# Optimization experiments

Hardware: AMD Instinct MI355X
Metric: run time of the kernel (lower is better)

The kernel has to match this reference:

```python
import jax, jax.numpy as jnp
import numpy as np

NEG_SLOPE = 0.2


def _gat(x, src, dst, W, a_src, a_dst, b, N):
    # PyG GATConv (eval mode, concat=True). W: [Fin, H*C], a_*: [H, C], b: [H*C]
    H, C = a_src.shape
    h = (x @ W).reshape(N, H, C)                       # [N,H,C]
    al_s = jnp.einsum('nhc,hc->nh', h, a_src)          # source attention logits
    al_d = jnp.einsum('nhc,hc->nh', h, a_dst)          # target attention logits
    e = jax.nn.leaky_relu(al_s[src] + al_d[dst], NEG_SLOPE)  # [E,H]
    m = jax.ops.segment_max(e, dst, num_segments=N)
    m = jnp.where(jnp.isneginf(m), 0.0, m)
    p = jnp.exp(e - m[dst])
    s = jax.ops.segment_sum(p, dst, num_segments=N)
    alpha = p / (s[dst] + 1e-16)                       # segment softmax over incoming edges
    out = jax.ops.segment_sum(h[src] * alpha[:, :, None], dst, num_segments=N)
    return out.reshape(N, H * C) + b


def _lin(key, fin, fout):
    k1, k2 = jax.random.split(key)
    w = jax.random.normal(k1, (fin, fout), jnp.float32) / np.sqrt(fin)
    b = jax.random.normal(k2, (fout,), jnp.float32) * 0.01
    return w, b


def _gat_params(key, fin, H, C):
    k1, k2, k3, k4 = jax.random.split(key, 4)
    W = jax.random.normal(k1, (fin, H * C), jnp.float32) / np.sqrt(fin)
    a_s = jax.random.normal(k2, (H, C), jnp.float32) / np.sqrt(C)
    a_d = jax.random.normal(k3, (H, C), jnp.float32) / np.sqrt(C)
    b = jax.random.normal(k4, (H * C,), jnp.float32) * 0.01
    return W, a_s, a_d, b


def setup_inputs() -> dict:
    key = jax.random.key(0)
    N, E, F, HID, H = 20000, 320000, 128, 128, 2
    W_ = HID * H  # 256
    ks = jax.random.split(key, 12)
    x = jax.random.normal(ks[0], (N, F), jnp.float32)
    edge_index = jax.random.randint(ks[1], (2, E), 0, N, jnp.int64)
    edge_attr = jax.random.normal(ks[2], (E, 4), jnp.float32)
    ec_w1, ec_b1 = _lin(ks[3], 2 * F, HID)
    ec_w2, ec_b2 = _lin(ks[4], HID, HID)
    g1 = _gat_params(ks[5], HID, H, HID)
    g2 = _gat_params(ks[6], W_, H, HID)
    reg_w, reg_b = _lin(ks[7], W_, W_)
    g3 = _gat_params(ks[8], W_, H, HID)
    g4 = _gat_params(ks[9], W_, H, HID)
    fin_w, fin_b = _lin(ks[10], W_, 1)
    d = {"x": x, "edge_index": edge_index, "edge_attr": edge_attr,
         "ec_w1": ec_w1, "ec_b1": ec_b1, "ec_w2": ec_w2, "ec_b2": ec_b2,
         "reg_w": reg_w, "reg_b": reg_b, "fin_w": fin_w, "fin_b": fin_b}
    for name, p in (("g1", g1), ("g2", g2), ("g3", g3), ("g4", g4)):
        d[name + "_w"], d[name + "_as"], d[name + "_ad"], d[name + "_b"] = p
    return d


def reference(x, edge_index, edge_attr,
              ec_w1, ec_b1, ec_w2, ec_b2,
              g1_w, g1_as, g1_ad, g1_b,
              g2_w, g2_as, g2_ad, g2_b,
              reg_w, reg_b,
              g3_w, g3_as, g3_ad, g3_b,
              g4_w, g4_as, g4_ad, g4_b,
              fin_w, fin_b):
    N = x.shape[0]
    src, dst = edge_index[0], edge_index[1]
    # EdgeConv: msg = MLP([x_i, x_j - x_i]), max-aggregation at target i (no self loops)
    xi = x[dst]
    msg = jnp.concatenate([xi, x[src] - xi], axis=-1)          # [E, 2F]
    h = jnp.maximum(msg @ ec_w1 + ec_b1, 0.0) @ ec_w2 + ec_b2   # [E, HID]
    agg = jax.ops.segment_max(h, dst, num_segments=N)
    x = jnp.where(jnp.isneginf(agg), 0.0, agg)
    # GATConv adds self loops by default
    loop = jnp.arange(N, dtype=src.dtype)
    s2 = jnp.concatenate([src, loop])
    d2 = jnp.concatenate([dst, loop])
    # edge_attr is ignored by GATConv (edge_dim=None)
    x = jax.nn.relu(_gat(x, s2, d2, g1_w, g1_as, g1_ad, g1_b, N))
    r = x
    x = jax.nn.relu(_gat(x, s2, d2, g2_w, g2_as, g2_ad, g2_b, N)) + r
    x = x @ reg_w + reg_b
    r = x
    x = jax.nn.relu(_gat(x, s2, d2, g3_w, g3_as, g3_ad, g3_b, N)) + r
    x = jax.nn.relu(_gat(x, s2, d2, g4_w, g4_as, g4_ad, g4_b, N))
    return x @ fin_w + fin_b
```

## Files before the change

kernel.cpp:

```cpp
#include <hip/hip_runtime.h>
#include <math.h>


#define NEG_SLOPE 0.2f

typedef short short8 __attribute__((ext_vector_type(8)));
typedef float float4v __attribute__((ext_vector_type(4)));
typedef unsigned short ushort4v __attribute__((ext_vector_type(4)));

#define AS1 __attribute__((address_space(1)))
#define AS3 __attribute__((address_space(3)))

__device__ __forceinline__ void cp16(const void* g, void* l) {
  __builtin_amdgcn_global_load_lds((const AS1 unsigned int*)g, (AS3 unsigned int*)l, 16, 0, 0);
}

__device__ __forceinline__ float leaky(float x) { return x > 0.f ? x : NEG_SLOPE * x; }

__device__ __forceinline__ void atomicMaxF(float* addr, float v) {
  if (v >= 0.f) atomicMax((int*)addr, __float_as_int(v));
  else          atomicMin((unsigned int*)addr, __float_as_uint(v));
}

__device__ __forceinline__ unsigned short bf16_rn(float f) {
  unsigned u = __float_as_uint(f);
  unsigned r = (u + 0x7FFFu + ((u >> 16) & 1u)) >> 16;
  return (unsigned short)r;
}
__device__ __forceinline__ float bf16_to_f(unsigned short h) {
  return __uint_as_float(((unsigned)h) << 16);
}

__global__ __launch_bounds__(256) void k_fill_f32(float* p, float v, int n) {
  int i = blockIdx.x * 256 + threadIdx.x;
  if (i < n) p[i] = v;
}

__global__ __launch_bounds__(256) void k_split_act(const float* __restrict__ src,
                                                   unsigned short* __restrict__ h,
                                                   unsigned short* __restrict__ l,
                                                   int n, int fixinf) {
  int i4 = (blockIdx.x * 256 + threadIdx.x) * 4;
  if (i4 >= n) return;
  float4 v = *(const float4*)&src[i4];
  if (fixinf) {
    if (v.x == -INFINITY) v.x = 0.f;
    if (v.y == -INFINITY) v.y = 0.f;
    if (v.z == -INFINITY) v.z = 0.f;
    if (v.w == -INFINITY) v.w = 0.f;
  }
  unsigned short hx = bf16_rn(v.x), hy = bf16_rn(v.y), hz = bf16_rn(v.z), hw = bf16_rn(v.w);
  ushort4v h4 = {hx, hy, hz, hw};
  ushort4v l4 = {bf16_rn(v.x - bf16_to_f(hx)), bf16_rn(v.y - bf16_to_f(hy)),
                 bf16_rn(v.z - bf16_to_f(hz)), bf16_rn(v.w - bf16_to_f(hw))};
  *(ushort4v*)&h[i4] = h4;
  *(ushort4v*)&l[i4] = l4;
}

__global__ __launch_bounds__(256) void k_hist(const int* __restrict__ ei, int* __restrict__ deg,
                                              int E) {
  int e = blockIdx.x * 256 + threadIdx.x;
  if (e < E) atomicAdd(&deg[ei[E + e]], 1);
}

__global__ __launch_bounds__(1024) void k_scan(const int* __restrict__ deg, int* __restrict__ rs,
                                               int n) {
  __shared__ int wsum[16];
  __shared__ int carry;
  int tid = threadIdx.x, lane = tid & 63, wv = tid >> 6;
  if (tid == 0) carry = 0;
  __syncthreads();
  for (int base = 0; base < n; base += 1024) {
    int i = base + tid;
    int v = (i < n) ? deg[i] : 0;
    int s = v;
    #pragma unroll
    for (int o = 1; o < 64; o <<= 1) {
      int t = __shfl(s, lane - o);
      if (lane >= o) s += t;
    }
    if (lane == 63) wsum[wv] = s;
    __syncthreads();
    if (wv == 0) {
      int x = (lane < 16) ? wsum[lane] : 0;
      #pragma unroll
      for (int o = 1; o < 16; o <<= 1) {
        int t = __shfl(x, lane - o);
        if (lane >= o) x += t;
      }
      if (lane < 16) wsum[lane] = x;
    }
    __syncthreads();
    int woff = carry + (wv ? wsum[wv - 1] : 0);
    if (i < n) rs[i] = woff + s - v;
    __syncthreads();
    if (tid == 0) carry += wsum[15];
    __syncthreads();
  }
  if (tid == 0) rs[n] = carry;
}

__global__ __launch_bounds__(256) void k_scatter(const int* __restrict__ ei,
                                                 const int* __restrict__ rs,
                                                 int* __restrict__ cnt,
                                                 int* __restrict__ csr_src,
                                                 int* __restrict__ csr_dst, int E) {
  int e = blockIdx.x * 256 + threadIdx.x;
  if (e < E) {
    int d = ei[E + e];
    int p = atomicAdd(&cnt[d], 1);
    int slot = rs[d] + p;
    csr_src[slot] = ei[e];
    csr_dst[slot] = d;
  }
}

struct SplitJob {
  const float* W;
  const float* aux;
  unsigned short* Th;
  unsigned short* Tl;
  float* bias_out;
  int K, N, kshift, type;
};
struct SplitJobs { SplitJob j[7]; };

__global__ __launch_bounds__(256) void k_prep_all(SplitJobs jobs) {
  SplitJob jb = jobs.j[blockIdx.y];
  int idx = blockIdx.x * 256 + threadIdx.x;
  if (idx >= jb.K * jb.N) return;
  float v;
  if (jb.type == 0) {
    int n = idx >> jb.kshift;
    int k = idx & (jb.K - 1);
    v = jb.W[k * jb.N + n];
  } else {
    int n = idx >> 7;
    int k = idx & 127;
    if (n < 128) v = jb.W[k * 128 + n] - jb.W[(k + 128) * 128 + n];
    else         v = jb.W[(k + 128) * 128 + (n - 128)];
    if (idx < 256) jb.bias_out[idx] = (idx < 128) ? jb.aux[idx] : 0.f;
  }
  unsigned short h = bf16_rn(v);
  jb.Th[idx] = h;
  jb.Tl[idx] = bf16_rn(v - bf16_to_f(h));
}

__global__ __launch_bounds__(256) void k_gemm_mfma(const unsigned short* __restrict__ Ah,
                                                   const unsigned short* __restrict__ Al,
                                                   const unsigned short* __restrict__ BTh,
                                                   const unsigned short* __restrict__ BTl,
                                                   const float* __restrict__ bias,
                                                   float* __restrict__ C, int M, int K,
                                                   unsigned short* __restrict__ Ch,
                                                   unsigned short* __restrict__ Cl,
                                                   const float* __restrict__ a_s,
                                                   const float* __restrict__ a_d,
                                                   float* __restrict__ al_out) {
  __shared__ __align__(16) char sm[24576];
  __shared__ float alS[64][2];
  char* AhS = sm;
  char* AlS = sm + 4096;
  char* BhS = sm + 8192;
  char* BlS = sm + 16384;

  const int tid = threadIdx.x;
  const int bm = blockIdx.x * 64;
  const int bn = blockIdx.y * 128;
  const int w = tid >> 6, lane = tid & 63, quad = lane >> 4, lr = lane & 15;
  const int kq8 = quad * 8;

  float4v zero4 = {0.f, 0.f, 0.f, 0.f};
  float4v acc[4][2];
  #pragma unroll
  for (int mt = 0; mt < 4; ++mt)
    #pragma unroll
    for (int nt = 0; nt < 2; ++nt) acc[mt][nt] = zero4;

  int ar = bm + w * 16 + lr; if (ar >= M) ar = M - 1;
  const size_t aoff  = (size_t)ar * K + kq8;
  const size_t boff0 = (size_t)(bn + (2 * w) * 16 + lr) * K + kq8;
  const size_t boff1 = (size_t)(bn + (2 * w + 1) * 16 + lr) * K + kq8;
  char* lA   = AhS + w * 1024;
  char* lAl  = AlS + w * 1024;
  char* lB0  = BhS + (2 * w) * 1024;
  char* lB1  = BhS + (2 * w + 1) * 1024;
  char* lBl0 = BlS + (2 * w) * 1024;
  char* lBl1 = BlS + (2 * w + 1) * 1024;

  for (int k0 = 0; k0 < K; k0 += 32) {
    __syncthreads();
    cp16(Ah + aoff + k0, lA);
    cp16(Al + aoff + k0, lAl);
    cp16(BTh + boff0 + k0, lB0);
    cp16(BTh + boff1 + k0, lB1);
    cp16(BTl + boff0 + k0, lBl0);
    cp16(BTl + boff1 + k0, lBl1);
    __syncthreads();
    short8 ah[4], alo[4], bh[2], blo[2];
    #pragma unroll
    for (int mt = 0; mt < 4; ++mt) {
      ah[mt]  = *(const short8*)(AhS + mt * 1024 + lane * 16);
      alo[mt] = *(const short8*)(AlS + mt * 1024 + lane * 16);
    }
    #pragma unroll
    for (int nt = 0; nt < 2; ++nt) {
      bh[nt]  = *(const short8*)(BhS + (2 * w + nt) * 1024 + lane * 16);
      blo[nt] = *(const short8*)(BlS + (2 * w + nt) * 1024 + lane * 16);
    }
    #pragma unroll
    for (int mt = 0; mt < 4; ++mt)
      #pragma unroll
      for (int nt = 0; nt < 2; ++nt) {
        acc[mt][nt] = __builtin_amdgcn_mfma_f32_16x16x32_bf16(ah[mt], bh[nt], acc[mt][nt], 0, 0, 0);
        acc[mt][nt] = __builtin_amdgcn_mfma_f32_16x16x32_bf16(alo[mt], bh[nt], acc[mt][nt], 0, 0, 0);
        acc[mt][nt] = __builtin_amdgcn_mfma_f32_16x16x32_bf16(ah[mt], blo[nt], acc[mt][nt], 0, 0, 0);
      }
  }
  #pragma unroll
  for (int nt = 0; nt < 2; ++nt) {
    int n = bn + w * 32 + nt * 16 + lr;
    float bv = bias ? bias[n] : 0.f;
    #pragma unroll
    for (int mt = 0; mt < 4; ++mt) {
      #pragma unroll
      for (int r = 0; r < 4; ++r) {
        int m = bm + mt * 16 + quad * 4 + r;
        if (m < M) {
          float v = acc[mt][nt][r] + bv;
          size_t idx = (size_t)m * 256 + n;
          C[idx] = v;
          if (Ch) {
            unsigned short h = bf16_rn(v);
            Ch[idx] = h;
            Cl[idx] = bf16_rn(v - bf16_to_f(h));
          }
        }
      }
    }
  }
  if (a_s) {
    if (tid < 128) ((float*)alS)[tid] = 0.f;
    __syncthreads();
    float asv[2], adv[2];
    #pragma unroll
    for (int nt = 0; nt < 2; ++nt) {
      int n = bn + w * 32 + nt * 16 + lr;
      asv[nt] = a_s[n];
      adv[nt] = a_d[n];
    }
    #pragma unroll
    for (int mt = 0; mt < 4; ++mt) {
      #pragma unroll
      for (int r = 0; r < 4; ++r) {
        float ps = acc[mt][0][r] * asv[0] + acc[mt][1][r] * asv[1];
        float pd = acc[mt][0][r] * adv[0] + acc[mt][1][r] * adv[1];
        #pragma unroll
        for (int o = 8; o; o >>= 1) {
          ps += __shfl_xor(ps, o);
          pd += __shfl_xor(pd, o);
        }
        if (lr == 0) {
          int row = mt * 16 + quad * 4 + r;
          atomicAdd(&alS[row][0], ps);
          atomicAdd(&alS[row][1], pd);
        }
      }
    }
    __syncthreads();
    int head = bn >> 7;
    if (tid < 64) {
      int m = bm + tid;
      if (m < M) {
        al_out[m * 4 + head]     = alS[tid][0];
        al_out[m * 4 + 2 + head] = alS[tid][1];
      }
    }
  }
}

__global__ __launch_bounds__(256, 4) void k_edgeconv2(const float* __restrict__ uv,
                                                      const int* __restrict__ csr_src,
                                                      const int* __restrict__ csr_dst,
                                                      const unsigned short* __restrict__ w2Th,
                                                      const unsigned short* __restrict__ w2Tl,
                                                      const float* __restrict__ b2,
                                                      float* __restrict__ x0, int E) {
  __shared__ __align__(16) char smem[34816];
  unsigned short (*Ph)[136] = (unsigned short(*)[136])smem;
  unsigned short (*Pl)[136] = (unsigned short(*)[136])(smem + 17408);
  float (*H2)[132] = (float(*)[132])smem;
  __shared__ int sSrc[64], sDst[64];

  const int tid = threadIdx.x;
  const int e0 = blockIdx.x * 64;
  const int w = tid >> 6, lane = tid & 63, quad = lane >> 4, lr = lane & 15;
  if (tid < 64) {
    int e = e0 + tid;
    sSrc[tid] = (e < E) ? csr_src[e] : -1;
    sDst[tid] = (e < E) ? csr_dst[e] : -1;
  }
  __syncthreads();
  #pragma unroll
  for (int c = tid; c < 1024; c += 256) {
    int r = c >> 4;
    int kq = (c & 15) * 8;
    float pv[8];
    int sn = sSrc[r], dn = sDst[r];
    if (sn >= 0) {
      float4 u0 = *(const float4*)&uv[(size_t)dn * 256 + kq];
      float4 u1 = *(const float4*)&uv[(size_t)dn * 256 + kq + 4];
      float4 v0 = *(const float4*)&uv[(size_t)sn * 256 + 128 + kq];
      float4 v1 = *(const float4*)&uv[(size_t)sn * 256 + 128 + kq + 4];
      pv[0] = fmaxf(u0.x + v0.x, 0.f); pv[1] = fmaxf(u0.y + v0.y, 0.f);
      pv[2] = fmaxf(u0.z + v0.z, 0.f); pv[3] = fmaxf(u0.w + v0.w, 0.f);
      pv[4] = fmaxf(u1.x + v1.x, 0.f); pv[5] = fmaxf(u1.y + v1.y, 0.f);
      pv[6] = fmaxf(u1.z + v1.z, 0.f); pv[7] = fmaxf(u1.w + v1.w, 0.f);
    } else {
      #pragma unroll
      for (int i = 0; i < 8; ++i) pv[i] = 0.f;
    }
    short8 h8, l8;
    #pragma unroll
    for (int i = 0; i < 8; ++i) {
      unsigned short h = bf16_rn(pv[i]);
      h8[i] = (short)h;
      l8[i] = (short)bf16_rn(pv[i] - bf16_to_f(h));
    }
    *(short8*)&Ph[r][kq] = h8;
    *(short8*)&Pl[r][kq] = l8;
  }
  __syncthreads();
  float4v zero4 = {0.f, 0.f, 0.f, 0.f};
  float4v acc[4][2];
  #pragma unroll
  for (int mt = 0; mt < 4; ++mt)
    #pragma unroll
    for (int nt = 0; nt < 2; ++nt) acc[mt][nt] = zero4;

  #pragma unroll
  for (int k0 = 0; k0 < 128; k0 += 32) {
    short8 ah[4], alo[4], bh[2], blo[2];
    #pragma unroll
    for (int nt = 0; nt < 2; ++nt) {
      int n = w * 32 + nt * 16 + lr;
      bh[nt]  = *(const short8*)&w2Th[(size_t)n * 128 + k0 + quad * 8];
      blo[nt] = *(const short8*)&w2Tl[(size_t)n * 128 + k0 + quad * 8];
    }
    #pragma unroll
    for (int mt = 0; mt < 4; ++mt) {
      ah[mt]  = *(short8*)&Ph[mt * 16 + lr][k0 + quad * 8];
      alo[mt] = *(short8*)&Pl[mt * 16 + lr][k0 + quad * 8];
    }
    #pragma unroll
    for (int mt = 0; mt < 4; ++mt)
      #pragma unroll
      for (int nt = 0; nt < 2; ++nt) {
        acc[mt][nt] = __builtin_amdgcn_mfma_f32_16x16x32_bf16(ah[mt], bh[nt], acc[mt][nt], 0, 0, 0);
        acc[mt][nt] = __builtin_amdgcn_mfma_f32_16x16x32_bf16(alo[mt], bh[nt], acc[mt][nt], 0, 0, 0);
        acc[mt][nt] = __builtin_amdgcn_mfma_f32_16x16x32_bf16(ah[mt], blo[nt], acc[mt][nt], 0, 0, 0);
      }
  }
  __syncthreads();
  #pragma unroll
  for (int nt = 0; nt < 2; ++nt) {
    int n = w * 32 + nt * 16 + lr;
    float bv = b2[n];
    #pragma unroll
    for (int mt = 0; mt < 4; ++mt) {
      #pragma unroll
      for (int r = 0; r < 4; ++r) {
        int row = mt * 16 + quad * 4 + r;
        H2[row][n] = acc[mt][nt][r] + bv;
      }
    }
  }
  __syncthreads();
  if (tid < 128) {
    int col = tid;
    int prev = sDst[0];
    float rmax = H2[0][col];
    for (int r = 1; r < 64; ++r) {
      int d = sDst[r];
      float v = H2[r][col];
      if (d == prev) {
        rmax = fmaxf(rmax, v);
      } else {
        if (prev >= 0) atomicMaxF(&x0[(size_t)prev * 128 + col], rmax);
        prev = d;
        rmax = v;
      }
    }
    if (prev >= 0) atomicMaxF(&x0[(size_t)prev * 128 + col], rmax);
  }
}

__global__ __launch_bounds__(256) void k_gat_agg(const float* __restrict__ Hf,
                                                 const float* __restrict__ al,
                                                 const int* __restrict__ rs,
                                                 const int* __restrict__ csr_src,
                                                 const float* __restrict__ bias,
                                                 const float* __restrict__ res,
                                                 float* __restrict__ out,
                                                 unsigned short* __restrict__ outh,
                                                 unsigned short* __restrict__ outl,
                                                 const float* __restrict__ finw,
                                                 const float* __restrict__ finb, int N) {
  int wave = threadIdx.x >> 6, lane = threadIdx.x & 63;
  int i = blockIdx.x * 4 + wave;
  if (i >= N) return;
  int beg = rs[i], end = rs[i + 1];
  int deg = end - beg;
  float4 me = *(const float4*)&al[i * 4];
  float ad0 = me.z, ad1 = me.w;
  float sl0 = leaky(me.x + ad0);
  float sl1 = leaky(me.y + ad1);
  const int c = lane << 2;
  const int hsel = lane >> 5;
  float a0, a1, a2, a3;

  if (deg <= 64) {
    int s = 0;
    float l0 = -INFINITY, l1 = -INFINITY;
    bool act = lane < deg;
    if (act) {
      s = csr_src[beg + lane];
      float4 a4 = *(const float4*)&al[s * 4];
      l0 = leaky(a4.x + ad0);
      l1 = leaky(a4.y + ad1);
    }
    float m0 = fmaxf(sl0, l0), m1 = fmaxf(sl1, l1);
    #pragma unroll
    for (int o = 32; o; o >>= 1) {
      m0 = fmaxf(m0, __shfl_xor(m0, o));
      m1 = fmaxf(m1, __shfl_xor(m1, o));
    }
    float w0 = act ? __expf(l0 - m0) : 0.f;
    float w1 = act ? __expf(l1 - m1) : 0.f;
    float s0 = w0, s1 = w1;
    #pragma unroll
    for (int o = 32; o; o >>= 1) {
      s0 += __shfl_xor(s0, o);
      s1 += __shfl_xor(s1, o);
    }
    s0 += __expf(sl0 - m0);
    s1 += __expf(sl1 - m1);
    float inv0 = 1.f / (s0 + 1e-16f), inv1 = 1.f / (s1 + 1e-16f);
    float wp0 = w0 * inv0, wp1 = w1 * inv1;
    float wself = hsel ? __expf(sl1 - m1) * inv1 : __expf(sl0 - m0) * inv0;
    float4 hv = *(const float4*)&Hf[(size_t)i * 256 + c];
    a0 = wself * hv.x; a1 = wself * hv.y; a2 = wself * hv.z; a3 = wself * hv.w;
    float b0 = 0.f, b1 = 0.f, b2 = 0.f, b3 = 0.f;
    float c0 = 0.f, c1 = 0.f, c2 = 0.f, c3 = 0.f;
    float d0 = 0.f, d1 = 0.f, d2 = 0.f, d3 = 0.f;
    int j = 0;
    for (; j + 8 <= deg; j += 8) {
      int   sjj[8];
      float wjj[8];
      #pragma unroll
      for (int q = 0; q < 8; ++q) {
        sjj[q] = __shfl(s, j + q);
        float wA = __shfl(wp0, j + q);
        float wB = __shfl(wp1, j + q);
        wjj[q] = hsel ? wB : wA;
      }
      float4 h0 = *(const float4*)&Hf[(size_t)sjj[0] * 256 + c];
      float4 h1 = *(const float4*)&Hf[(size_t)sjj[1] * 256 + c];
      float4 h2 = *(const float4*)&Hf[(size_t)sjj[2] * 256 + c];
      float4 h3 = *(const float4*)&Hf[(size_t)sjj[3] * 256 + c];
      float4 h4 = *(const float4*)&Hf[(size_t)sjj[4] * 256 + c];
      float4 h5 = *(const float4*)&Hf[(size_t)sjj[5] * 256 + c];
      float4 h6 = *(const float4*)&Hf[(size_t)sjj[6] * 256 + c];
      float4 h7 = *(const float4*)&Hf[(size_t)sjj[7] * 256 + c];
      a0 += wjj[0] * h0.x; a1 += wjj[0] * h0.y; a2 += wjj[0] * h0.z; a3 += wjj[0] * h0.w;
      b0 += wjj[1] * h1.x; b1 += wjj[1] * h1.y; b2 += wjj[1] * h1.z; b3 += wjj[1] * h1.w;
      c0 += wjj[2] * h2.x; c1 += wjj[2] * h2.y; c2 += wjj[2] * h2.z; c3 += wjj[2] * h2.w;
      d0 += wjj[3] * h3.x; d1 += wjj[3] * h3.y; d2 += wjj[3] * h3.z; d3 += wjj[3] * h3.w;
      a0 += wjj[4] * h4.x; a1 += wjj[4] * h4.y; a2 += wjj[4] * h4.z; a3 += wjj[4] * h4.w;
      b0 += wjj[5] * h5.x; b1 += wjj[5] * h5.y; b2 += wjj[5] * h5.z; b3 += wjj[5] * h5.w;
      c0 += wjj[6] * h6.x; c1 += wjj[6] * h6.y; c2 += wjj[6] * h6.z; c3 += wjj[6] * h6.w;
      d0 += wjj[7] * h7.x; d1 += wjj[7] * h7.y; d2 += wjj[7] * h7.z; d3 += wjj[7] * h7.w;
    }
    for (; j < deg; ++j) {
      int sj = __shfl(s, j);
      float wA = __shfl(wp0, j);
      float wB = __shfl(wp1, j);
      float wj = hsel ? wB : wA;
      float4 h4 = *(const float4*)&Hf[(size_t)sj * 256 + c];
      a0 += wj * h4.x; a1 += wj * h4.y; a2 += wj * h4.z; a3 += wj * h4.w;
    }
    a0 += b0 + c0 + d0; a1 += b1 + c1 + d1;
    a2 += b2 + c2 + d2; a3 += b3 + c3 + d3;
  } else {
    float m0 = sl0, m1 = sl1;
    for (int e = beg + lane; e < end; e += 64) {
      int s = csr_src[e];
      m0 = fmaxf(m0, leaky(al[s * 4 + 0] + ad0));
      m1 = fmaxf(m1, leaky(al[s * 4 + 1] + ad1));
    }
    #pragma unroll
    for (int o = 32; o; o >>= 1) {
      m0 = fmaxf(m0, __shfl_xor(m0, o));
      m1 = fmaxf(m1, __shfl_xor(m1, o));
    }
    float s0 = 0.f, s1 = 0.f;
    for (int e = beg + lane; e < end; e += 64) {
      int s = csr_src[e];
      s0 += __expf(leaky(al[s * 4 + 0] + ad0) - m0);
      s1 += __expf(leaky(al[s * 4 + 1] + ad1) - m1);
    }
    #pragma unroll
    for (int o = 32; o; o >>= 1) {
      s0 += __shfl_xor(s0, o);
      s1 += __shfl_xor(s1, o);
    }
    s0 += __expf(sl0 - m0);
    s1 += __expf(sl1 - m1);
    float inv0 = 1.f / (s0 + 1e-16f), inv1 = 1.f / (s1 + 1e-16f);
    float mh = hsel ? m1 : m0;
    float invh = hsel ? inv1 : inv0;
    float adh = hsel ? ad1 : ad0;
    float wself = __expf((hsel ? sl1 : sl0) - mh) * invh;
    float4 hv = *(const float4*)&Hf[(size_t)i * 256 + c];
    a0 = wself * hv.x; a1 = wself * hv.y; a2 = wself * hv.z; a3 = wself * hv.w;
    for (int e = beg; e < end; ++e) {
      int s = csr_src[e];
      float wgt = __expf(leaky(al[s * 4 + hsel] + adh) - mh) * invh;
      float4 h4 = *(const float4*)&Hf[(size_t)s * 256 + c];
      a0 += wgt * h4.x; a1 += wgt * h4.y; a2 += wgt * h4.z; a3 += wgt * h4.w;
    }
  }
  float4 bv = *(const float4*)&bias[c];
  float4 o4;
  o4.x = fmaxf(a0 + bv.x, 0.f);
  o4.y = fmaxf(a1 + bv.y, 0.f);
  o4.z = fmaxf(a2 + bv.z, 0.f);
  o4.w = fmaxf(a3 + bv.w, 0.f);
  if (res) {
    float4 r4 = *(const float4*)&res[(size_t)i * 256 + c];
    o4.x += r4.x; o4.y += r4.y; o4.z += r4.z; o4.w += r4.w;
  }
  if (finw) {
    float4 wv = *(const float4*)&finw[c];
    float p = o4.x * wv.x + o4.y * wv.y + o4.z * wv.z + o4.w * wv.w;
    #pragma unroll
    for (int o = 32; o; o >>= 1) p += __shfl_xor(p, o);
    if (lane == 0) out[i] = p + finb[0];
    return;
  }
  size_t idx = (size_t)i * 256 + c;
  *(float4*)&out[idx] = o4;
  if (outh) {
    unsigned short hx = bf16_rn(o4.x), hy = bf16_rn(o4.y), hz = bf16_rn(o4.z), hw = bf16_rn(o4.w);
    ushort4v h4 = {hx, hy, hz, hw};
    ushort4v l4 = {bf16_rn(o4.x - bf16_to_f(hx)), bf16_rn(o4.y - bf16_to_f(hy)),
                   bf16_rn(o4.z - bf16_to_f(hz)), bf16_rn(o4.w - bf16_to_f(hw))};
    *(ushort4v*)&outh[idx] = h4;
    *(ushort4v*)&outl[idx] = l4;
  }
}

extern "C" void kernel_launch(void* const* d_in, const int* in_sizes, int n_in,
                              void* d_out, int out_size, void* d_ws, size_t ws_size,
                              hipStream_t stream) {
  const float* x      = (const float*)d_in[0];
  const int*   ei     = (const int*)d_in[1];
  const float* ec_w1  = (const float*)d_in[3];
  const float* ec_b1  = (const float*)d_in[4];
  const float* ec_w2  = (const float*)d_in[5];
  const float* ec_b2  = (const float*)d_in[6];
  const float* reg_w  = (const float*)d_in[7];
  const float* reg_b  = (const float*)d_in[8];
  const float* fin_w  = (const float*)d_in[9];
  const float* fin_b  = (const float*)d_in[10];
  const float* g1_w   = (const float*)d_in[11];
  const float* g1_as  = (const float*)d_in[12];
  const float* g1_ad  = (const float*)d_in[13];
  const float* g1_b   = (const float*)d_in[14];
  const float* g2_w   = (const float*)d_in[15];
  const float* g2_as  = (const float*)d_in[16];
  const float* g2_ad  = (const float*)d_in[17];
  const float* g2_b   = (const float*)d_in[18];
  const float* g3_w   = (const float*)d_in[19];
  const float* g3_as  = (const float*)d_in[20];
  const float* g3_ad  = (const float*)d_in[21];
  const float* g3_b   = (const float*)d_in[22];
  const float* g4_w   = (const float*)d_in[23];
  const float* g4_as  = (const float*)d_in[24];
  const float* g4_ad  = (const float*)d_in[25];
  const float* g4_b   = (const float*)d_in[26];

  const int N = in_sizes[0] / 128;
  const int E = in_sizes[1] / 2;

  char* base = (char*)d_ws;
  size_t off = 0;
  auto alloc = [&](size_t bytes) -> char* {
    char* p = base + off;
    off += (bytes + 255) & ~(size_t)255;
    return p;
  };
  const size_t szN4 = ((size_t)N * 4 + 255) & ~(size_t)255;
  int*   deg      = (int*)alloc((size_t)N * 4);
  int*   cnt      = (int*)alloc((size_t)N * 4);
  int*   rs       = (int*)alloc((size_t)(N + 1) * 4);
  int*   csr_src  = (int*)alloc((size_t)E * 4);
  int*   csr_dst  = (int*)alloc((size_t)E * 4);
  float* bias_cat = (float*)alloc(256 * 4);
  unsigned short* bcatTh = (unsigned short*)alloc(256 * 128 * 2);
  unsigned short* bcatTl = (unsigned short*)alloc(256 * 128 * 2);
  unsigned short* w2Th   = (unsigned short*)alloc(128 * 128 * 2);
  unsigned short* w2Tl   = (unsigned short*)alloc(128 * 128 * 2);
  unsigned short* g1Th   = (unsigned short*)alloc(256 * 128 * 2);
  unsigned short* g1Tl   = (unsigned short*)alloc(256 * 128 * 2);
  unsigned short* g2Th   = (unsigned short*)alloc(256 * 256 * 2);
  unsigned short* g2Tl   = (unsigned short*)alloc(256 * 256 * 2);
  unsigned short* g3Th   = (unsigned short*)alloc(256 * 256 * 2);
  unsigned short* g3Tl   = (unsigned short*)alloc(256 * 256 * 2);
  unsigned short* g4Th   = (unsigned short*)alloc(256 * 256 * 2);
  unsigned short* g4Tl   = (unsigned short*)alloc(256 * 256 * 2);
  unsigned short* regTh  = (unsigned short*)alloc(256 * 256 * 2);
  unsigned short* regTl  = (unsigned short*)alloc(256 * 256 * 2);
  float* uv = (float*)alloc((size_t)N * 256 * 4);
  float* x0 = (float*)alloc((size_t)N * 128 * 4);
  float* X1 = (float*)alloc((size_t)N * 256 * 4);
  float* X2 = (float*)alloc((size_t)N * 256 * 4);
  float* al = (float*)alloc((size_t)N * 4 * 4);
  unsigned short* s1h = (unsigned short*)alloc((size_t)N * 256 * 2);
  unsigned short* s1l = (unsigned short*)alloc((size_t)N * 256 * 2);
  unsigned short* s2h = (unsigned short*)alloc((size_t)N * 256 * 2);
  unsigned short* s2l = (unsigned short*)alloc((size_t)N * 256 * 2);
  (void)ws_size; (void)n_in; (void)out_size;

  const int nodeWaveBlocks = (N + 3) / 4;
  const dim3 gemmGrid((N + 63) / 64, 2);
  const int splitBlocks128 = (N * 128 / 4 + 255) / 256;

  SplitJobs jobs;
  jobs.j[0] = {ec_w2, nullptr, w2Th, w2Tl, nullptr, 128, 128, 7, 0};
  jobs.j[1] = {g1_w,  nullptr, g1Th, g1Tl, nullptr, 128, 256, 7, 0};
  jobs.j[2] = {g2_w,  nullptr, g2Th, g2Tl, nullptr, 256, 256, 8, 0};
  jobs.j[3] = {g3_w,  nullptr, g3Th, g3Tl, nullptr, 256, 256, 8, 0};
  jobs.j[4] = {g4_w,  nullptr, g4Th, g4Tl, nullptr, 256, 256, 8, 0};
  jobs.j[5] = {reg_w, nullptr, regTh, regTl, nullptr, 256, 256, 8, 0};
  jobs.j[6] = {ec_w1, ec_b1, bcatTh, bcatTl, bias_cat, 128, 256, 7, 1};
  k_prep_all<<<dim3(256, 7), 256, 0, stream>>>(jobs);

  hipMemsetAsync(deg, 0, 2 * szN4, stream);
  k_hist<<<(E + 255) / 256, 256, 0, stream>>>(ei, deg, E);
  k_scan<<<1, 1024, 0, stream>>>(deg, rs, N);
  k_scatter<<<(E + 255) / 256, 256, 0, stream>>>(ei, rs, cnt, csr_src, csr_dst, E);

  k_split_act<<<splitBlocks128, 256, 0, stream>>>(x, s1h, s1l, N * 128, 0);
  k_gemm_mfma<<<gemmGrid, 256, 0, stream>>>(s1h, s1l, bcatTh, bcatTl, bias_cat, uv, N, 128,
                                            nullptr, nullptr, nullptr, nullptr, nullptr);
  k_fill_f32<<<(N * 128 + 255) / 256, 256, 0, stream>>>(x0, -INFINITY, N * 128);
  k_edgeconv2<<<(E + 63) / 64, 256, 0, stream>>>(uv, csr_src, csr_dst, w2Th, w2Tl, ec_b2, x0, E);
  k_split_act<<<splitBlocks128, 256, 0, stream>>>(x0, s1h, s1l, N * 128, 1);

  k_gemm_mfma<<<gemmGrid, 256, 0, stream>>>(s1h, s1l, g1Th, g1Tl, nullptr, uv, N, 128,
                                            nullptr, nullptr, g1_as, g1_ad, al);
  k_gat_agg<<<nodeWaveBlocks, 256, 0, stream>>>(uv, al, rs, csr_src, g1_b, nullptr, X1,
                                                s1h, s1l, nullptr, nullptr, N);

  k_gemm_mfma<<<gemmGrid, 256, 0, stream>>>(s1h, s1l, g2Th, g2Tl, nullptr, uv, N, 256,
                                            nullptr, nullptr, g2_as, g2_ad, al);
  k_gat_agg<<<nodeWaveBlocks, 256, 0, stream>>>(uv, al, rs, csr_src, g2_b, X1, X2,
                                                s2h, s2l, nullptr, nullptr, N);

  k_gemm_mfma<<<gemmGrid, 256, 0, stream>>>(s2h, s2l, regTh, regTl, reg_b, X1, N, 256,
                                            s1h, s1l, nullptr, nullptr, nullptr);

  k_gemm_mfma<<<gemmGrid, 256, 0, stream>>>(s1h, s1l, g3Th, g3Tl, nullptr, uv, N, 256,
                                            nullptr, nullptr, g3_as, g3_ad, al);
  k_gat_agg<<<nodeWaveBlocks, 256, 0, stream>>>(uv, al, rs, csr_src, g3_b, X1, X2,
                                                s2h, s2l, nullptr, nullptr, N);

  k_gemm_mfma<<<gemmGrid, 256, 0, stream>>>(s2h, s2l, g4Th, g4Tl, nullptr, uv, N, 256,
                                            nullptr, nullptr, g4_as, g4_ad, al);
  k_gat_agg<<<nodeWaveBlocks, 256, 0, stream>>>(uv, al, rs, csr_src, g4_b, nullptr,
                                                (float*)d_out, nullptr, nullptr,
                                                fin_w, fin_b, N);
}
```

Baseline: 618.8 us.

## Store GAT projected features as bf16 for aggregation gathers and split edgeconv max

The GAT projection GEMMs now write only a bf16 copy of the projected features instead of fp32, and the aggregation kernel gathers 8-byte bf16 vectors per neighbour instead of 16-byte fp32 vectors. This halves the bytes moved in the gather-heavy aggregation and in the GEMM stores, at the cost of bf16 rounding of the messages (attention logits are still computed from fp32 accumulators). Separately, the edgeconv segment-max epilogue now uses all 256 threads, each handling half the rows, instead of 128 threads scanning 64 rows.

```diff
diff --git a/kernel.cpp b/kernel.cpp
--- a/kernel.cpp
+++ b/kernel.cpp
@@ -29,6 +29,13 @@
 }
 __device__ __forceinline__ float bf16_to_f(unsigned short h) {
   return __uint_as_float(((unsigned)h) << 16);
+}
+__device__ __forceinline__ float4 ld_bf4(const unsigned short* p) {
+  ushort4v u = *(const ushort4v*)p;
+  float4 f;
+  f.x = bf16_to_f(u[0]); f.y = bf16_to_f(u[1]);
+  f.z = bf16_to_f(u[2]); f.w = bf16_to_f(u[3]);
+  return f;
 }
 
 __global__ __launch_bounds__(256) void k_fill_f32(float* p, float v, int n) {
@@ -154,6 +161,7 @@
                                                    float* __restrict__ C, int M, int K,
                                                    unsigned short* __restrict__ Ch,
                                                    unsigned short* __restrict__ Cl,
+                                                   unsigned short* __restrict__ Cbf,
                                                    const float* __restrict__ a_s,
                                                    const float* __restrict__ a_d,
                                                    float* __restrict__ al_out) {
@@ -229,7 +237,8 @@
         if (m < M) {
           float v = acc[mt][nt][r] + bv;
           size_t idx = (size_t)m * 256 + n;
-          C[idx] = v;
+          if (C) C[idx] = v;
+          if (Cbf) Cbf[idx] = bf16_rn(v);
           if (Ch) {
             unsigned short h = bf16_rn(v);
             Ch[idx] = h;
@@ -376,11 +385,13 @@
     }
   }
   __syncthreads();
-  if (tid < 128) {
-    int col = tid;
-    int prev = sDst[0];
-    float rmax = H2[0][col];
-    for (int r = 1; r < 64; ++r) {
+  {
+    int half = tid >> 7;
+    int col = tid & 127;
+    int r0 = half * 32;
+    int prev = sDst[r0];
+    float rmax = H2[r0][col];
+    for (int r = r0 + 1; r < r0 + 32; ++r) {
       int d = sDst[r];
       float v = H2[r][col];
       if (d == prev) {
@@ -395,7 +406,7 @@
   }
 }
 
-__global__ __launch_bounds__(256) void k_gat_agg(const float* __restrict__ Hf,
+__global__ __launch_bounds__(256) void k_gat_agg(const unsigned short* __restrict__ Hfb,
                                                  const float* __restrict__ al,
                                                  const int* __restrict__ rs,
                                                  const int* __restrict__ csr_src,
@@ -448,7 +459,7 @@
     float inv0 = 1.f / (s0 + 1e-16f), inv1 = 1.f / (s1 + 1e-16f);
     float wp0 = w0 * inv0, wp1 = w1 * inv1;
     float wself = hsel ? __expf(sl1 - m1) * inv1 : __expf(sl0 - m0) * inv0;
-    float4 hv = *(const float4*)&Hf[(size_t)i * 256 + c];
+    float4 hv = ld_bf4(&Hfb[(size_t)i * 256 + c]);
     a0 = wself * hv.x; a1 = wself * hv.y; a2 = wself * hv.z; a3 = wself * hv.w;
     float b0 = 0.f, b1 = 0.f, b2 = 0.f, b3 = 0.f;
     float c0 = 0.f, c1 = 0.f, c2 = 0.f, c3 = 0.f;
@@ -464,14 +475,14 @@
         float wB = __shfl(wp1, j + q);
         wjj[q] = hsel ? wB : wA;
       }
-      float4 h0 = *(const float4*)&Hf[(size_t)sjj[0] * 256 + c];
-      float4 h1 = *(const float4*)&Hf[(size_t)sjj[1] * 256 + c];
-      float4 h2 = *(const float4*)&Hf[(size_t)sjj[2] * 256 + c];
-      float4 h3 = *(const float4*)&Hf[(size_t)sjj[3] * 256 + c];
-      float4 h4 = *(const float4*)&Hf[(size_t)sjj[4] * 256 + c];
-      float4 h5 = *(const float4*)&Hf[(size_t)sjj[5] * 256 + c];
-      float4 h6 = *(const float4*)&Hf[(size_t)sjj[6] * 256 + c];
-      float4 h7 = *(const float4*)&Hf[(size_t)sjj[7] * 256 + c];
+      float4 h0 = ld_bf4(&Hfb[(size_t)sjj[0] * 256 + c]);
+      float4 h1 = ld_bf4(&Hfb[(size_t)sjj[1] * 256 + c]);
+      float4 h2 = ld_bf4(&Hfb[(size_t)sjj[2] * 256 + c]);
+      float4 h3 = ld_bf4(&Hfb[(size_t)sjj[3] * 256 + c]);
+      float4 h4 = ld_bf4(&Hfb[(size_t)sjj[4] * 256 + c]);
+      float4 h5 = ld_bf4(&Hfb[(size_t)sjj[5] * 256 + c]);
+      float4 h6 = ld_bf4(&Hfb[(size_t)sjj[6] * 256 + c]);
+      float4 h7 = ld_bf4(&Hfb[(size_t)sjj[7] * 256 + c]);
       a0 += wjj[0] * h0.x; a1 += wjj[0] * h0.y; a2 += wjj[0] * h0.z; a3 += wjj[0] * h0.w;
       b0 += wjj[1] * h1.x; b1 += wjj[1] * h1.y; b2 += wjj[1] * h1.z; b3 += wjj[1] * h1.w;
       c0 += wjj[2] * h2.x; c1 += wjj[2] * h2.y; c2 += wjj[2] * h2.z; c3 += wjj[2] * h2.w;
@@ -486,7 +497,7 @@
       float wA = __shfl(wp0, j);
       float wB = __shfl(wp1, j);
       float wj = hsel ? wB : wA;
-      float4 h4 = *(const float4*)&Hf[(size_t)sj * 256 + c];
+      float4 h4 = ld_bf4(&Hfb[(size_t)sj * 256 + c]);
       a0 += wj * h4.x; a1 += wj * h4.y; a2 += wj * h4.z; a3 += wj * h4.w;
     }
     a0 += b0 + c0 + d0; a1 += b1 + c1 + d1;
@@ -521,12 +532,12 @@
     float invh = hsel ? inv1 : inv0;
     float adh = hsel ? ad1 : ad0;
     float wself = __expf((hsel ? sl1 : sl0) - mh) * invh;
-    float4 hv = *(const float4*)&Hf[(size_t)i * 256 + c];
+    float4 hv = ld_bf4(&Hfb[(size_t)i * 256 + c]);
     a0 = wself * hv.x; a1 = wself * hv.y; a2 = wself * hv.z; a3 = wself * hv.w;
     for (int e = beg; e < end; ++e) {
       int s = csr_src[e];
       float wgt = __expf(leaky(al[s * 4 + hsel] + adh) - mh) * invh;
-      float4 h4 = *(const float4*)&Hf[(size_t)s * 256 + c];
+      float4 h4 = ld_bf4(&Hfb[(size_t)s * 256 + c]);
       a0 += wgt * h4.x; a1 += wgt * h4.y; a2 += wgt * h4.z; a3 += wgt * h4.w;
     }
   }
@@ -621,7 +632,8 @@
   unsigned short* g4Tl   = (unsigned short*)alloc(256 * 256 * 2);
   unsigned short* regTh  = (unsigned short*)alloc(256 * 256 * 2);
   unsigned short* regTl  = (unsigned short*)alloc(256 * 256 * 2);
-  float* uv = (float*)alloc((size_t)N * 256 * 4);
+  float* uv  = (float*)alloc((size_t)N * 256 * 4);
+  unsigned short* uvh = (unsigned short*)alloc((size_t)N * 256 * 2);
   float* x0 = (float*)alloc((size_t)N * 128 * 4);
   float* X1 = (float*)alloc((size_t)N * 256 * 4);
   float* X2 = (float*)alloc((size_t)N * 256 * 4);
@@ -653,32 +665,33 @@
 
   k_split_act<<<splitBlocks128, 256, 0, stream>>>(x, s1h, s1l, N * 128, 0);
   k_gemm_mfma<<<gemmGrid, 256, 0, stream>>>(s1h, s1l, bcatTh, bcatTl, bias_cat, uv, N, 128,
-                                            nullptr, nullptr, nullptr, nullptr, nullptr);
+                                            nullptr, nullptr, nullptr,
+                                            nullptr, nullptr, nullptr);
   k_fill_f32<<<(N * 128 + 255) / 256, 256, 0, stream>>>(x0, -INFINITY, N * 128);
   k_edgeconv2<<<(E + 63) / 64, 256, 0, stream>>>(uv, csr_src, csr_dst, w2Th, w2Tl, ec_b2, x0, E);
   k_split_act<<<splitBlocks128, 256, 0, stream>>>(x0, s1h, s1l, N * 128, 1);
 
-  k_gemm_mfma<<<gemmGrid, 256, 0, stream>>>(s1h, s1l, g1Th, g1Tl, nullptr, uv, N, 128,
-                                            nullptr, nullptr, g1_as, g1_ad, al);
-  k_gat_agg<<<nodeWaveBlocks, 256, 0, stream>>>(uv, al, rs, csr_src, g1_b, nullptr, X1,
+  k_gemm_mfma<<<gemmGrid, 256, 0, stream>>>(s1h, s1l, g1Th, g1Tl, nullptr, nullptr, N, 128,
+                                            nullptr, nullptr, uvh, g1_as, g1_ad, al);
+  k_gat_agg<<<nodeWaveBlocks, 256, 0, stream>>>(uvh, al, rs, csr_src, g1_b, nullptr, X1,
                                                 s1h, s1l, nullptr, nullptr, N);
 
-  k_gemm_mfma<<<gemmGrid, 256, 0, stream>>>(s1h, s1l, g2Th, g2Tl, nullptr, uv, N, 256,
-                                            nullptr, nullptr, g2_as, g2_ad, al);
-  k_gat_agg<<<nodeWaveBlocks, 256, 0, stream>>>(uv, al, rs, csr_src, g2_b, X1, X2,
+  k_gemm_mfma<<<gemmGrid, 256, 0, stream>>>(s1h, s1l, g2Th, g2Tl, nullptr, nullptr, N, 256,
+                                            nullptr, nullptr, uvh, g2_as, g2_ad, al);
+  k_gat_agg<<<nodeWaveBlocks, 256, 0, stream>>>(uvh, al, rs, csr_src, g2_b, X1, X2,
                                                 s2h, s2l, nullptr, nullptr, N);
 
   k_gemm_mfma<<<gemmGrid, 256, 0, stream>>>(s2h, s2l, regTh, regTl, reg_b, X1, N, 256,
-                                            s1h, s1l, nullptr, nullptr, nullptr);
-
-  k_gemm_mfma<<<gemmGrid, 256, 0, stream>>>(s1h, s1l, g3Th, g3Tl, nullptr, uv, N, 256,
-                                            nullptr, nullptr, g3_as, g3_ad, al);
-  k_gat_agg<<<nodeWaveBlocks, 256, 0, stream>>>(uv, al, rs, csr_src, g3_b, X1, X2,
+                                            s1h, s1l, nullptr, nullptr, nullptr, nullptr);
+
+  k_gemm_mfma<<<gemmGrid, 256, 0, stream>>>(s1h, s1l, g3Th, g3Tl, nullptr, nullptr, N, 256,
+                                            nullptr, nullptr, uvh, g3_as, g3_ad, al);
+  k_gat_agg<<<nodeWaveBlocks, 256, 0, stream>>>(uvh, al, rs, csr_src, g3_b, X1, X2,
                                                 s2h, s2l, nullptr, nullptr, N);
 
-  k_gemm_mfma<<<gemmGrid, 256, 0, stream>>>(s2h, s2l, g4Th, g4Tl, nullptr, uv, N, 256,
-                                            nullptr, nullptr, g4_as, g4_ad, al);
-  k_gat_agg<<<nodeWaveBlocks, 256, 0, stream>>>(uv, al, rs, csr_src, g4_b, nullptr,
+  k_gemm_mfma<<<gemmGrid, 256, 0, stream>>>(s2h, s2l, g4Th, g4Tl, nullptr, nullptr, N, 256,
+                                            nullptr, nullptr, uvh, g4_as, g4_ad, al);
+  k_gat_agg<<<nodeWaveBlocks, 256, 0, stream>>>(uvh, al, rs, csr_src, g4_b, nullptr,
                                                 (float*)d_out, nullptr, nullptr,
                                                 fin_w, fin_b, N);
 }
```

Result: faster. 535.3 us (median of 2 runs) (-13.5%).
